# Kernel tuning notes

Hardware: AMD Instinct MI355X
Metric: run time of the kernel (lower is better)

## Reference

```python
import jax, jax.numpy as jnp
import numpy as np

N = 30000        # nodes
E = 600000       # edges
R = 32           # relations
NB = 30          # num_bases
D = 128          # entity_dim == hidden_dim == output_dim
H = 8            # heads, head dim C = D // H = 16
NUM_ENT = 100000
NGRAPH = 16      # graphs in batch
L = 2            # num_rgcn_layers == num_transformer_layers
EPS = 1e-5


def _ln(x, g, b):
    mu = x.mean(-1, keepdims=True)
    var = ((x - mu) ** 2).mean(-1, keepdims=True)
    return (x - mu) * jax.lax.rsqrt(var + EPS) * g + b


def setup_inputs() -> dict:
    key = jax.random.key(0)
    ks = iter(jax.random.split(key, 48))

    def nrm(shape, s=0.05):
        return jax.random.normal(next(ks), shape, jnp.float32) * s

    inp = {}
    inp["node_ids"] = jax.random.randint(next(ks), (N,), 0, NUM_ENT)
    inp["edge_index"] = jax.random.randint(next(ks), (2, E), 0, N)
    inp["edge_type"] = jax.random.randint(next(ks), (E,), 0, R)
    inp["batch"] = jnp.sort(jax.random.randint(next(ks), (N,), 0, NGRAPH))
    inp["entity_emb"] = nrm((NUM_ENT, D)).at[0].set(0.0)  # padding_idx=0
    inp["rel_emb"] = nrm((R, D)).at[0].set(0.0)           # padding_idx=0
    inp["rgcn_comp"] = nrm((L, R, NB))
    inp["rgcn_bases"] = nrm((L, NB, D, D))
    inp["rgcn_root"] = nrm((L, D, D))
    inp["rgcn_bias"] = jnp.zeros((L, D), jnp.float32)
    inp["rgcn_ln_g"] = jnp.ones((L, D), jnp.float32)
    inp["rgcn_ln_b"] = jnp.zeros((L, D), jnp.float32)
    inp["tr_wq"] = nrm((L, D, D)); inp["tr_bq"] = jnp.zeros((L, D), jnp.float32)
    inp["tr_wk"] = nrm((L, D, D)); inp["tr_bk"] = jnp.zeros((L, D), jnp.float32)
    inp["tr_wv"] = nrm((L, D, D)); inp["tr_bv"] = jnp.zeros((L, D), jnp.float32)
    inp["tr_we"] = nrm((L, D, D))                          # lin_edge (bias=False in PyG)
    inp["tr_wskip"] = nrm((L, D, D)); inp["tr_bskip"] = jnp.zeros((L, D), jnp.float32)
    inp["tr_ln_g"] = jnp.ones((L, D), jnp.float32)
    inp["tr_ln_b"] = jnp.zeros((L, D), jnp.float32)
    return inp


def reference(node_ids, edge_index, edge_type, batch, entity_emb, rel_emb,
              rgcn_comp, rgcn_bases, rgcn_root, rgcn_bias, rgcn_ln_g, rgcn_ln_b,
              tr_wq, tr_bq, tr_wk, tr_bk, tr_wv, tr_bv, tr_we, tr_wskip, tr_bskip,
              tr_ln_g, tr_ln_b):
    src, tgt = edge_index[0], edge_index[1]
    C = D // H
    x = entity_emb[node_ids]            # [N, D]
    edge_attr = rel_emb[edge_type]      # [E, D]

    # ---- RGCN layers: basis decomposition, mean aggregation per (target, relation) ----
    seg = tgt * R + edge_type
    cnt = jax.ops.segment_sum(jnp.ones((E,), jnp.float32), seg, num_segments=N * R)
    inv = jnp.where(cnt > 0, 1.0 / jnp.maximum(cnt, 1.0), 0.0)   # [N*R]
    for l in range(L):
        agg = jax.ops.segment_sum(x[src], seg, num_segments=N * R)   # [N*R, D]
        agg = (agg * inv[:, None]).reshape(N, R, D)
        w = jnp.einsum('rb,bio->rio', rgcn_comp[l], rgcn_bases[l])   # [R, D, D]
        x = jnp.einsum('nri,rio->no', agg, w) + x @ rgcn_root[l] + rgcn_bias[l]
        x = jax.nn.relu(_ln(x, rgcn_ln_g[l], rgcn_ln_b[l]))          # dropout = identity (eval)

    # ---- TransformerConv layers: edge-conditioned multi-head attention ----
    for l in range(L):
        q = (x @ tr_wq[l] + tr_bq[l]).reshape(N, H, C)
        k = (x @ tr_wk[l] + tr_bk[l]).reshape(N, H, C)
        v = (x @ tr_wv[l] + tr_bv[l]).reshape(N, H, C)
        e = (edge_attr @ tr_we[l]).reshape(E, H, C)
        kj = k[src] + e                                              # [E, H, C]
        vj = v[src] + e
        alpha = jnp.einsum('ehc,ehc->eh', q[tgt], kj) / np.float32(np.sqrt(C))
        m = jax.ops.segment_max(alpha, tgt, num_segments=N)          # [N, H]
        a = jnp.exp(alpha - m[tgt])
        denom = jax.ops.segment_sum(a, tgt, num_segments=N)
        a = a / jnp.maximum(denom[tgt], 1e-16)                       # softmax per target node
        out = jax.ops.segment_sum((vj * a[:, :, None]).reshape(E, D), tgt, num_segments=N)
        out = out + x @ tr_wskip[l] + tr_bskip[l]                    # root/skip connection
        out = jax.nn.relu(_ln(out, tr_ln_g[l], tr_ln_b[l]))          # dropout = identity (eval)
        x = x + out                                                  # dims match -> residual

    cnt_g = jax.ops.segment_sum(jnp.ones((N,), jnp.float32), batch, num_segments=NGRAPH)
    graph_emb = jax.ops.segment_sum(x, batch, num_segments=NGRAPH) / jnp.maximum(cnt_g, 1.0)[:, None]
    return x, graph_emb
```

## Files before the change

kernel.cpp:

```cpp
#include <hip/hip_runtime.h>

#define NN 30000
#define NE 600000
#define RR 32
#define NBASE 30
#define NG 16

typedef long long i64;
typedef unsigned short ushort;
typedef short bf16x8 __attribute__((ext_vector_type(8)));
typedef float f32x4 __attribute__((ext_vector_type(4)));

__device__ __forceinline__ ushort f2bf(float f){
  unsigned u = __float_as_uint(f);
  u += 0x7fffu + ((u >> 16) & 1u);
  return (ushort)(u >> 16);
}
__device__ __forceinline__ float bf2f(ushort u){
  return __uint_as_float(((unsigned)u) << 16);
}
__device__ __forceinline__ unsigned pk2(float a, float b){
  return (unsigned)f2bf(a) | ((unsigned)f2bf(b) << 16);
}

__global__ void k_gather(const float* __restrict__ emb, const int* __restrict__ ids,
                         float* __restrict__ x, ushort* __restrict__ xb){
  int t = blockIdx.x*256 + threadIdx.x;
  if (t >= NN*32) return;
  int n = t >> 5, c = t & 31;
  float4 v = ((const float4*)emb)[(i64)ids[n]*32 + c];
  ((float4*)x)[(i64)n*32 + c] = v;
  *(uint2*)&xb[(i64)n*128 + c*4] = make_uint2(pk2(v.x, v.y), pk2(v.z, v.w));
}

__global__ void k_cnt(const int* __restrict__ tgt, const int* __restrict__ ety,
                      float* __restrict__ cnt){
  int e = blockIdx.x*256 + threadIdx.x;
  if (e >= NE) return;
  atomicAdd(&cnt[(i64)tgt[e]*RR + ety[e]], 1.0f);
}

__global__ void k_hist_blk(const int* __restrict__ ety, int* __restrict__ hist){
  __shared__ int lh[RR];
  if (threadIdx.x < RR) lh[threadIdx.x] = 0;
  __syncthreads();
  int e0 = blockIdx.x*2048 + threadIdx.x;
  #pragma unroll
  for (int i = 0; i < 8; i++){
    int e = e0 + i*256;
    if (e < NE) atomicAdd(&lh[ety[e]], 1);
  }
  __syncthreads();
  if (threadIdx.x < RR){
    int v = lh[threadIdx.x];
    if (v) atomicAdd(&hist[threadIdx.x], v);
  }
}

__global__ void k_scan(const int* __restrict__ hist, int* __restrict__ base,
                       int* __restrict__ cursor, int* __restrict__ pb,
                       int* __restrict__ pb64){
  if (threadIdx.x != 0 || blockIdx.x != 0) return;
  int s = 0, p = 0, p64 = 0;
  for (int r = 0; r < RR; r++){
    base[r] = s; cursor[r] = s; pb[r] = p; pb64[r] = p64;
    s += hist[r]; p += (hist[r] + 127) >> 7; p64 += (hist[r] + 63) >> 6;
  }
  base[RR] = s; pb[RR] = p; pb64[RR] = p64;
}

__global__ __launch_bounds__(256) void k_scatter_blk(const int* __restrict__ ety,
    int* __restrict__ cursor, int* __restrict__ eord){
  __shared__ int lh[RR];
  __shared__ int lb[RR];
  if (threadIdx.x < RR) lh[threadIdx.x] = 0;
  __syncthreads();
  int e0 = blockIdx.x*2048 + threadIdx.x;
  #pragma unroll
  for (int i = 0; i < 8; i++){
    int e = e0 + i*256;
    if (e < NE) atomicAdd(&lh[ety[e]], 1);
  }
  __syncthreads();
  if (threadIdx.x < RR){
    int c = lh[threadIdx.x];
    lb[threadIdx.x] = c ? atomicAdd(&cursor[threadIdx.x], c) : 0;
  }
  __syncthreads();
  if (threadIdx.x < RR) lh[threadIdx.x] = 0;
  __syncthreads();
  #pragma unroll
  for (int i = 0; i < 8; i++){
    int e = e0 + i*256;
    if (e < NE){
      int r = ety[e];
      int loc = atomicAdd(&lh[r], 1);
      eord[lb[r] + loc] = e;
    }
  }
}

__global__ void k_hist2(const int* __restrict__ etgt, int* __restrict__ hist2){
  int e = blockIdx.x*256 + threadIdx.x;
  if (e >= NE) return;
  atomicAdd(&hist2[etgt[e]], 1);
}

__global__ __launch_bounds__(1024) void k_scan2(const int* __restrict__ hist2,
    int* __restrict__ rowptr, int* __restrict__ cursor2){
  __shared__ int s[1024];
  int t = threadIdx.x;
  int base = t*30;
  int loc[30];
  int sum = 0;
  #pragma unroll
  for (int i = 0; i < 30; i++){
    int v = (base+i < NN) ? hist2[base+i] : 0;
    loc[i] = sum; sum += v;
  }
  s[t] = sum; __syncthreads();
  for (int off = 1; off < 1024; off <<= 1){
    int v = (t >= off) ? s[t-off] : 0;
    __syncthreads();
    s[t] += v;
    __syncthreads();
  }
  int excl = (t > 0) ? s[t-1] : 0;
  #pragma unroll
  for (int i = 0; i < 30; i++){
    int idx = base + i;
    if (idx <= NN){
      rowptr[idx] = excl + loc[i];
      if (idx < NN) cursor2[idx] = excl + loc[i];
    }
  }
}

__global__ void k_scatter2(const int* __restrict__ etgt, const int* __restrict__ esrc,
                           const int* __restrict__ ety, int* __restrict__ cursor2,
                           int2* __restrict__ se2, int* __restrict__ pos2){
  int e = blockIdx.x*256 + threadIdx.x;
  if (e >= NE) return;
  int q = atomicAdd(&cursor2[etgt[e]], 1);
  se2[q] = make_int2(esrc[e], ety[e]);
  pos2[e] = q;
}

__global__ void k_prep(const int* __restrict__ eord, const int* __restrict__ esrc,
                       const int* __restrict__ etgt, const int* __restrict__ ety,
                       const int* __restrict__ pos2, const float* __restrict__ cnt,
                       int* __restrict__ sg_src, int* __restrict__ sg_p2,
                       float* __restrict__ sg_inv){
  int s = blockIdx.x*256 + threadIdx.x;
  if (s >= NE) return;
  int eid = eord[s];
  sg_src[s] = esrc[eid];
  sg_p2[s]  = pos2[eid];
  sg_inv[s] = 1.0f / cnt[(i64)etgt[eid]*RR + ety[eid]];
}

__global__ void k_basis(const float* __restrict__ comp, const float* __restrict__ bases,
                        float* __restrict__ wT, ushort* __restrict__ wTb){
  int t = blockIdx.x*256 + threadIdx.x;
  int r = t >> 14, rem = t & 16383, c = rem >> 7, kk = rem & 127;
  float acc = 0.f;
  for (int b = 0; b < NBASE; b++)
    acc += comp[r*NBASE + b] * bases[(i64)b*16384 + kk*128 + c];
  wT[t] = acc;
  wTb[t] = f2bf(acc);
}

__global__ void k_tw(const float* __restrict__ root, const float* __restrict__ wq,
                     const float* __restrict__ wk, const float* __restrict__ wv,
                     const float* __restrict__ wsk, ushort* __restrict__ out){
  int z = blockIdx.y;
  const float* srcs[5] = {root, wq, wk, wv, wsk};
  const float* S = srcs[z >> 1] + (i64)(z & 1)*16384;
  int idx = blockIdx.x*256 + threadIdx.x;
  int c = idx >> 7, kk = idx & 127;
  out[(i64)z*16384 + idx] = f2bf(S[kk*128 + c]);
}


__global__ __launch_bounds__(256, 4) void k_mm_mfma(const ushort* __restrict__ xb,
    const ushort* __restrict__ wTb, const float* __restrict__ bias,
    float* __restrict__ Y, int nrows){
  __shared__ ushort Xs[16384];
  int t = threadIdx.x;
  int row0 = blockIdx.x * 128;
  for (int i = t; i < 2048; i += 256){
    int row = i >> 4, c = i & 15;
    int gr = min(row0 + row, nrows - 1);
    *(uint4*)((char*)Xs + row*256 + ((c*16) ^ ((row&7)<<4))) =
        *(const uint4*)((const char*)(xb + (i64)gr*128) + c*16);
  }
  __syncthreads();
  int w = t >> 6, l = t & 63;
  int wm = w >> 1, wn = w & 1;
  int lrow = l & 15, lg = l >> 4;
  int swz = (lrow & 7) << 4;
  const char* pX = (const char*)Xs + (wm*64 + lrow)*256;
  const char* pW = (const char*)wTb + (wn*64 + lrow)*256 + 16*lg;
  f32x4 acc[4][4] = {};
  #pragma unroll
  for (int ks = 0; ks < 4; ks++){
    int kb = (16*lg + 64*ks) ^ swz;
    bf16x8 a[4], bx[4];
    #pragma unroll
    for (int ns = 0; ns < 4; ns++) a[ns]  = *(const bf16x8*)(pW + ns*4096 + 64*ks);
    #pragma unroll
    for (int ms = 0; ms < 4; ms++) bx[ms] = *(const bf16x8*)(pX + ms*4096 + kb);
    #pragma unroll
    for (int ms = 0; ms < 4; ms++)
      #pragma unroll
      for (int ns = 0; ns < 4; ns++)
        acc[ms][ns] = __builtin_amdgcn_mfma_f32_16x16x32_bf16(a[ns], bx[ms], acc[ms][ns], 0, 0, 0);
  }
  #pragma unroll
  for (int ms = 0; ms < 4; ms++){
    int m = row0 + wm*64 + ms*16 + lrow;
    if (m >= nrows) continue;
    #pragma unroll
    for (int ns = 0; ns < 4; ns++){
      int n0 = wn*64 + ns*16 + 4*lg;
      float4 bv = *(const float4*)&bias[n0];
      f32x4 v = acc[ms][ns];
      *(float4*)&Y[(i64)m*128 + n0] =
          make_float4(v[0]+bv.x, v[1]+bv.y, v[2]+bv.z, v[3]+bv.w);
    }
  }
}

__global__ __launch_bounds__(256, 4) void k_mm4(const ushort* __restrict__ xb,
    const ushort* __restrict__ wTb, int layer,
    const float* __restrict__ biq, const float* __restrict__ bik,
    const float* __restrict__ biv, const float* __restrict__ bisk,
    ushort* __restrict__ qo, ushort* __restrict__ ko, ushort* __restrict__ vo,
    float* __restrict__ z, int nrows){
  __shared__ ushort Xs[16384];
  int t = threadIdx.x;
  int row0 = blockIdx.x * 128;
  for (int i = t; i < 2048; i += 256){
    int row = i >> 4, c = i & 15;
    int gr = min(row0 + row, nrows - 1);
    *(uint4*)((char*)Xs + row*256 + ((c*16) ^ ((row&7)<<4))) =
        *(const uint4*)((const char*)(xb + (i64)gr*128) + c*16);
  }
  __syncthreads();
  int w = t >> 6, l = t & 63;
  int wm = w >> 1, wn = w & 1;
  int lrow = l & 15, lg = l >> 4;
  int swz = (lrow & 7) << 4;
  const char* pX = (const char*)Xs + (wm*64 + lrow)*256;
  const float* biases[4] = {biq, bik, biv, bisk};
  ushort* outs[3] = {qo, ko, vo};
  #pragma unroll 1
  for (int arr = 0; arr < 4; arr++){
    const char* pW = (const char*)(wTb + (i64)(2 + 2*arr + layer)*16384)
                     + (wn*64 + lrow)*256 + 16*lg;
    f32x4 acc[4][4] = {};
    #pragma unroll
    for (int ks = 0; ks < 4; ks++){
      int kb = (16*lg + 64*ks) ^ swz;
      bf16x8 a[4], bx[4];
      #pragma unroll
      for (int ns = 0; ns < 4; ns++) a[ns]  = *(const bf16x8*)(pW + ns*4096 + 64*ks);
      #pragma unroll
      for (int ms = 0; ms < 4; ms++) bx[ms] = *(const bf16x8*)(pX + ms*4096 + kb);
      #pragma unroll
      for (int ms = 0; ms < 4; ms++)
        #pragma unroll
        for (int ns = 0; ns < 4; ns++)
          acc[ms][ns] = __builtin_amdgcn_mfma_f32_16x16x32_bf16(a[ns], bx[ms], acc[ms][ns], 0, 0, 0);
    }
    const float* bias = biases[arr];
    #pragma unroll
    for (int ms = 0; ms < 4; ms++){
      int m = row0 + wm*64 + ms*16 + lrow;
      if (m >= nrows) continue;
      #pragma unroll
      for (int ns = 0; ns < 4; ns++){
        int n0 = wn*64 + ns*16 + 4*lg;
        float4 bv = *(const float4*)&bias[n0];
        f32x4 v = acc[ms][ns];
        if (arr < 3){
          *(uint2*)&outs[arr][(i64)m*128 + n0] =
              make_uint2(pk2(v[0]+bv.x, v[1]+bv.y), pk2(v[2]+bv.z, v[3]+bv.w));
        } else {
          *(float4*)&z[(i64)m*128 + n0] =
              make_float4(v[0]+bv.x, v[1]+bv.y, v[2]+bv.z, v[3]+bv.w);
        }
      }
    }
  }
}

__global__ __launch_bounds__(256, 4) void k_edge_mfma(
    const int* __restrict__ sg_src, const int* __restrict__ sg_p2,
    const float* __restrict__ sg_inv, const int* __restrict__ hist,
    const int* __restrict__ base, const int* __restrict__ pb,
    const ushort* __restrict__ xb, const ushort* __restrict__ wb,
    ushort* __restrict__ y){
  __shared__ ushort Xs[16384];
  __shared__ int s_src[128];
  __shared__ int s_p2[128];
  __shared__ float s_inv[128];
  int b = blockIdx.x;
  int r = -1;
  #pragma unroll 1
  for (int i = 0; i < RR; i++){
    if (b >= pb[i] && b < pb[i+1]) { r = i; break; }
  }
  if (r < 0) return;
  int chunk = b - pb[r];
  int rowbase = base[r] + chunk*128;
  int nvalid = min(128, hist[r] - chunk*128);
  int t = threadIdx.x;
  if (t < 128){
    bool valid = t < nvalid;
    int slot = rowbase + (valid ? t : 0);
    s_src[t] = sg_src[slot];
    s_p2[t]  = valid ? sg_p2[slot] : NE;
    s_inv[t] = valid ? sg_inv[slot] : 0.0f;
  }
  __syncthreads();
  for (int i = t; i < 2048; i += 256){
    int row = i >> 4, c = i & 15;
    *(uint4*)((char*)Xs + row*256 + ((c*16) ^ ((row&7)<<4))) =
        *(const uint4*)((const char*)(xb + (i64)s_src[row]*128) + c*16);
  }
  __syncthreads();
  int w = t >> 6, l = t & 63;
  int wm = w >> 1, wn = w & 1;
  int lrow = l & 15, lg = l >> 4;
  int swz = (lrow & 7) << 4;
  const char* pX = (const char*)Xs + (wm*64 + lrow)*256;
  const char* pW = (const char*)(wb + (i64)r*16384) + (wn*64 + lrow)*256 + 16*lg;
  f32x4 acc[4][4] = {};
  #pragma unroll
  for (int ks = 0; ks < 4; ks++){
    int kb = (16*lg + 64*ks) ^ swz;
    bf16x8 a[4], bx[4];
    #pragma unroll
    for (int ns = 0; ns < 4; ns++) a[ns]  = *(const bf16x8*)(pW + ns*4096 + 64*ks);
    #pragma unroll
    for (int ms = 0; ms < 4; ms++) bx[ms] = *(const bf16x8*)(pX + ms*4096 + kb);
    #pragma unroll
    for (int ms = 0; ms < 4; ms++)
      #pragma unroll
      for (int ns = 0; ns < 4; ns++)
        acc[ms][ns] = __builtin_amdgcn_mfma_f32_16x16x32_bf16(a[ns], bx[ms], acc[ms][ns], 0, 0, 0);
  }
  __syncthreads();
  #pragma unroll
  for (int ms = 0; ms < 4; ms++){
    int m = wm*64 + ms*16 + lrow;
    float sc = s_inv[m];
    int msk = (m & 7) << 4;
    #pragma unroll
    for (int ns = 0; ns < 4; ns++){
      int n0 = wn*64 + ns*16 + 4*lg;
      f32x4 v = acc[ms][ns];
      *(uint2*)((char*)Xs + m*256 + ((n0*2) ^ msk)) =
          make_uint2(pk2(v[0]*sc, v[1]*sc), pk2(v[2]*sc, v[3]*sc));
    }
  }
  __syncthreads();
  for (int i = t; i < 2048; i += 256){
    int row = i >> 4, c = i & 15;
    uint4 v = *(const uint4*)((const char*)Xs + row*256 + ((c*16) ^ ((row&7)<<4)));
    *(uint4*)&y[(i64)s_p2[row]*128 + c*8] = v;
  }
}

__global__ __launch_bounds__(256) void k_edge_atomic(const int* __restrict__ esrc,
    const int* __restrict__ etgt, const int* __restrict__ eord,
    const int* __restrict__ hist, const int* __restrict__ base,
    const int* __restrict__ pb, const float* __restrict__ cnt,
    const float* __restrict__ x, const float* __restrict__ wT,
    float* __restrict__ z){
  __shared__ float Xs[64][132];
  __shared__ int s_src[64];
  __shared__ int s_tgt[64];
  __shared__ float s_inv[64];
  int b = blockIdx.x;
  int r = -1;
  #pragma unroll 1
  for (int i = 0; i < RR; i++){
    if (b >= pb[i] && b < pb[i+1]) { r = i; break; }
  }
  if (r < 0) return;
  int chunk = b - pb[r];
  int rowbase = base[r] + chunk*64;
  int cnt_r = hist[r];
  if (threadIdx.x < 64){
    int i = threadIdx.x;
    bool valid = (chunk*64 + i) < cnt_r;
    int eid = valid ? eord[rowbase + i] : 0;
    int sv = valid ? esrc[eid] : 0;
    int tv = valid ? etgt[eid] : 0;
    s_src[i] = sv; s_tgt[i] = tv;
    s_inv[i] = valid ? (1.0f / cnt[(i64)tv*RR + r]) : 0.0f;
  }
  __syncthreads();
  for (int idx = threadIdx.x; idx < 64*32; idx += 256){
    int rr = idx >> 5, c4 = idx & 31;
    *(float4*)&Xs[rr][c4*4] = ((const float4*)x)[(i64)s_src[rr]*32 + c4];
  }
  __syncthreads();
  const float* W = wT + (i64)r*16384;
  int m = threadIdx.x & 15, cg = threadIdx.x >> 4;
  float acc[4][8] = {};
  #pragma unroll 2
  for (int k4 = 0; k4 < 128; k4 += 4){
    float4 xv[4], wv[8];
    #pragma unroll
    for (int i = 0; i < 4; i++) xv[i] = *(float4*)&Xs[m + 16*i][k4];
    #pragma unroll
    for (int j = 0; j < 8; j++) wv[j] = *(const float4*)&W[(i64)(cg + 16*j)*128 + k4];
    #pragma unroll
    for (int i = 0; i < 4; i++)
      #pragma unroll
      for (int j = 0; j < 8; j++)
        acc[i][j] += xv[i].x*wv[j].x + xv[i].y*wv[j].y + xv[i].z*wv[j].z + xv[i].w*wv[j].w;
  }
  #pragma unroll
  for (int i = 0; i < 4; i++){
    int rr = m + 16*i;
    float sc = s_inv[rr];
    i64 o = (i64)s_tgt[rr]*128;
    #pragma unroll
    for (int j = 0; j < 8; j++)
      atomicAdd(&z[o + cg + 16*j], acc[i][j]*sc);
  }
}

__global__ void k_seg(const int* __restrict__ rowptr, const ushort* __restrict__ y,
                      const float* __restrict__ z, const float* __restrict__ g,
                      const float* __restrict__ b, float* __restrict__ x,
                      ushort* __restrict__ xb){
  int t = (blockIdx.x*256 + threadIdx.x) >> 6;
  int l = threadIdx.x & 63;
  if (t >= NN) return;
  int q0 = rowptr[t], q1 = rowptr[t+1];
  float ax = 0.f, ay = 0.f;
  for (int q = q0; q < q1; q++){
    ushort2 u = *(const ushort2*)&y[(i64)q*128 + 2*l];
    ax += bf2f(u.x); ay += bf2f(u.y);
  }
  float2 zv = *(const float2*)&z[(i64)t*128 + 2*l];
  float tx = ax + zv.x, ty = ay + zv.y;
  float s = tx + ty;
  #pragma unroll
  for (int o = 1; o < 64; o <<= 1) s += __shfl_xor(s, o);
  float mu = s * 0.0078125f;
  float dx = tx - mu, dy = ty - mu;
  float s2 = dx*dx + dy*dy;
  #pragma unroll
  for (int o = 1; o < 64; o <<= 1) s2 += __shfl_xor(s2, o);
  float rs = rsqrtf(s2 * 0.0078125f + 1e-5f);
  float2 gg = *(const float2*)&g[2*l];
  float2 bb = *(const float2*)&b[2*l];
  float o0 = fmaxf(dx*rs*gg.x + bb.x, 0.f);
  float o1 = fmaxf(dy*rs*gg.y + bb.y, 0.f);
  *(float2*)&x[(i64)t*128 + 2*l] = make_float2(o0, o1);
  *(unsigned*)&xb[(i64)t*128 + 2*l] = pk2(o0, o1);
}

__global__ void k_lnrelu(const float* __restrict__ z, const float* __restrict__ g,
                         const float* __restrict__ b, float* __restrict__ xo,
                         ushort* __restrict__ xb){
  int w = (blockIdx.x*256 + threadIdx.x) >> 6;
  int l = threadIdx.x & 63;
  if (w >= NN) return;
  float2 v = *(const float2*)&z[(i64)w*128 + 2*l];
  float s = v.x + v.y;
  #pragma unroll
  for (int o = 1; o < 64; o <<= 1) s += __shfl_xor(s, o);
  float mu = s * 0.0078125f;
  float dx = v.x - mu, dy = v.y - mu;
  float s2 = dx*dx + dy*dy;
  #pragma unroll
  for (int o = 1; o < 64; o <<= 1) s2 += __shfl_xor(s2, o);
  float rs = rsqrtf(s2 * 0.0078125f + 1e-5f);
  float2 gg = *(const float2*)&g[2*l];
  float2 bb = *(const float2*)&b[2*l];
  float o0 = fmaxf(dx*rs*gg.x + bb.x, 0.f);
  float o1 = fmaxf(dy*rs*gg.y + bb.y, 0.f);
  *(float2*)&xo[(i64)w*128 + 2*l] = make_float2(o0, o1);
  *(unsigned*)&xb[(i64)w*128 + 2*l] = pk2(o0, o1);
}

__global__ void k_ew(const float* __restrict__ rel, const float* __restrict__ we,
                     float* __restrict__ ew){
  int t = blockIdx.x*256 + threadIdx.x;
  int r = t >> 7, c = t & 127;
  float acc = 0.f;
  for (int k = 0; k < 128; k++) acc += rel[r*128 + k] * we[k*128 + c];
  ew[t] = acc;
}

__global__ __launch_bounds__(256) void k_attn(const int2* __restrict__ se2,
    const int* __restrict__ rowptr,
    const ushort* __restrict__ qbb, const ushort* __restrict__ kbb,
    const ushort* __restrict__ vbb, const float* __restrict__ ew,
    const float* __restrict__ sk, const float* __restrict__ g,
    const float* __restrict__ b, float* __restrict__ x, ushort* __restrict__ xb){
  __shared__ float sew[RR*128];
  for (int i = threadIdx.x; i < RR*32; i += 256)
    ((float4*)sew)[i] = ((const float4*)ew)[i];
  __syncthreads();
  int t = (blockIdx.x*256 + threadIdx.x) >> 6;
  int l = threadIdx.x & 63;
  if (t >= NN) return;
  int q0 = rowptr[t], q1 = rowptr[t+1];
  unsigned qu = *(const unsigned*)&qbb[(i64)t*128 + 2*l];
  float qx = bf2f((ushort)qu), qy = bf2f((ushort)(qu >> 16));
  float m = -3.0e38f, den = 0.f, ox = 0.f, oy = 0.f;
  if (q0 < q1){
    int2 sr = se2[q0];
    unsigned ku = *(const unsigned*)&kbb[(i64)sr.x*128 + 2*l];
    unsigned vu = *(const unsigned*)&vbb[(i64)sr.x*128 + 2*l];
    int r = sr.y;
    for (int q = q0; q < q1; q++){
      unsigned kun = 0, vun = 0; int rn = 0;
      if (q + 1 < q1){
        int2 srn = se2[q+1];
        kun = *(const unsigned*)&kbb[(i64)srn.x*128 + 2*l];
        vun = *(const unsigned*)&vbb[(i64)srn.x*128 + 2*l];
        rn = srn.y;
      }
      float2 ev = *(const float2*)&sew[r*128 + 2*l];
      float kx = bf2f((ushort)ku) + ev.x, ky = bf2f((ushort)(ku >> 16)) + ev.y;
      float p = qx*kx + qy*ky;
      p += __shfl_xor(p, 1); p += __shfl_xor(p, 2); p += __shfl_xor(p, 4);
      p *= 0.25f;
      float mn = fmaxf(m, p);
      float scl = __expf(m - mn);
      float wgt = __expf(p - mn);
      den = den*scl + wgt;
      ox = ox*scl + wgt*(bf2f((ushort)vu) + ev.x);
      oy = oy*scl + wgt*(bf2f((ushort)(vu >> 16)) + ev.y);
      m = mn;
      ku = kun; vu = vun; r = rn;
    }
  }
  float dn = fmaxf(den, 1e-16f);
  float2 zv = *(const float2*)&sk[(i64)t*128 + 2*l];
  float tx = ox/dn + zv.x, ty = oy/dn + zv.y;
  float s = tx + ty;
  #pragma unroll
  for (int o = 1; o < 64; o <<= 1) s += __shfl_xor(s, o);
  float mu = s * 0.0078125f;
  float dx = tx - mu, dy = ty - mu;
  float s2 = dx*dx + dy*dy;
  #pragma unroll
  for (int o = 1; o < 64; o <<= 1) s2 += __shfl_xor(s2, o);
  float rs = rsqrtf(s2 * 0.0078125f + 1e-5f);
  float2 gg = *(const float2*)&g[2*l];
  float2 bb = *(const float2*)&b[2*l];
  float o0 = fmaxf(dx*rs*gg.x + bb.x, 0.f);
  float o1 = fmaxf(dy*rs*gg.y + bb.y, 0.f);
  float2 xv = *(const float2*)&x[(i64)t*128 + 2*l];
  float nx = xv.x + o0, ny = xv.y + o1;
  *(float2*)&x[(i64)t*128 + 2*l] = make_float2(nx, ny);
  *(unsigned*)&xb[(i64)t*128 + 2*l] = pk2(nx, ny);
}

__global__ void k_copy(const float* __restrict__ x, float* __restrict__ out){
  int t = blockIdx.x*256 + threadIdx.x;
  if (t >= NN*32) return;
  ((float4*)out)[t] = ((const float4*)x)[t];
}

__global__ void k_cntg(const int* __restrict__ batch, float* __restrict__ cntg){
  __shared__ int lh[NG];
  if (threadIdx.x < NG) lh[threadIdx.x] = 0;
  __syncthreads();
  int n = blockIdx.x*256 + threadIdx.x;
  if (n < NN) atomicAdd(&lh[batch[n]], 1);
  __syncthreads();
  if (threadIdx.x < NG){
    int v = lh[threadIdx.x];
    if (v) atomicAdd(&cntg[threadIdx.x], (float)v);
  }
}

__global__ void k_pool(const float* __restrict__ x, const int* __restrict__ batch,
                       float* __restrict__ gsum){
  __shared__ float acc[NG*128];
  for (int i = threadIdx.x; i < NG*128; i += 256) acc[i] = 0.f;
  __syncthreads();
  int per = (NN + gridDim.x - 1) / gridDim.x;
  int n0 = blockIdx.x*per, n1 = min(n0 + per, NN);
  int sub = threadIdx.x >> 5, c4 = threadIdx.x & 31;
  for (int n = n0 + sub; n < n1; n += 8){
    int g = batch[n];
    float4 xv = ((const float4*)x)[(i64)n*32 + c4];
    atomicAdd(&acc[g*128 + c4*4 + 0], xv.x);
    atomicAdd(&acc[g*128 + c4*4 + 1], xv.y);
    atomicAdd(&acc[g*128 + c4*4 + 2], xv.z);
    atomicAdd(&acc[g*128 + c4*4 + 3], xv.w);
  }
  __syncthreads();
  for (int i = threadIdx.x; i < NG*128; i += 256) atomicAdd(&gsum[i], acc[i]);
}

__global__ void k_poolfin(const float* __restrict__ gsum, const float* __restrict__ cntg,
                          float* __restrict__ gout){
  int t = blockIdx.x*256 + threadIdx.x;
  int g = t >> 7;
  gout[t] = gsum[t] / fmaxf(cntg[g], 1.0f);
}

extern "C" void kernel_launch(void* const* d_in, const int* in_sizes, int n_in,
                              void* d_out, int out_size, void* d_ws, size_t ws_size,
                              hipStream_t stream) {
  const int*   node_ids = (const int*)d_in[0];
  const int*   eidx  = (const int*)d_in[1];
  const int*   esrc  = eidx;
  const int*   etgt  = eidx + NE;
  const int*   ety   = (const int*)d_in[2];
  const int*   batch = (const int*)d_in[3];
  const float* ent   = (const float*)d_in[4];
  const float* rel   = (const float*)d_in[5];
  const float* comp  = (const float*)d_in[6];
  const float* bases = (const float*)d_in[7];
  const float* root  = (const float*)d_in[8];
  const float* rbias = (const float*)d_in[9];
  const float* rlng  = (const float*)d_in[10];
  const float* rlnb  = (const float*)d_in[11];
  const float* wq    = (const float*)d_in[12];
  const float* bq    = (const float*)d_in[13];
  const float* wk    = (const float*)d_in[14];
  const float* bk    = (const float*)d_in[15];
  const float* wv    = (const float*)d_in[16];
  const float* bv    = (const float*)d_in[17];
  const float* we    = (const float*)d_in[18];
  const float* wsk   = (const float*)d_in[19];
  const float* bsk   = (const float*)d_in[20];
  const float* tlng  = (const float*)d_in[21];
  const float* tlnb  = (const float*)d_in[22];
  float* out = (float*)d_out;

  char* wp = (char*)d_ws;
  auto alloc = [&](size_t bytes)->void*{
    void* p = (void*)wp;
    wp += (bytes + 255) & ~(size_t)255;
    return p;
  };
  float*    x     = (float*)alloc((size_t)NN*128*4);
  ushort*   xb    = (ushort*)alloc((size_t)NN*128*2);
  float*    z     = (float*)alloc((size_t)NN*128*4);
  ushort*   qbb   = (ushort*)alloc((size_t)NN*128*2);
  ushort*   kbb   = (ushort*)alloc((size_t)NN*128*2);
  ushort*   vbb   = (ushort*)alloc((size_t)NN*128*2);
  float*    cnt   = (float*)alloc((size_t)NN*RR*4);
  float*    wbT   = (float*)alloc((size_t)RR*16384*4);
  ushort*   wbTb  = (ushort*)alloc((size_t)RR*16384*2);
  ushort*   wTb   = (ushort*)alloc((size_t)10*16384*2);
  float*    ew    = (float*)alloc((size_t)RR*128*4);
  int*      eord  = (int*)alloc((size_t)NE*4);
  int*      pos2  = (int*)alloc((size_t)NE*4);
  int2*     se2   = (int2*)alloc((size_t)NE*8);
  int*      sg_src= (int*)alloc((size_t)NE*4);
  int*      sg_p2 = (int*)alloc((size_t)NE*4);
  float*    sg_inv= (float*)alloc((size_t)NE*4);
  int*      hist  = (int*)alloc(RR*4);
  int*      base  = (int*)alloc((RR+1)*4);
  int*      cursor= (int*)alloc(RR*4);
  int*      pb    = (int*)alloc((RR+1)*4);
  int*      pb64  = (int*)alloc((RR+1)*4);
  int*      hist2 = (int*)alloc((size_t)NN*4);
  int*      rowptr= (int*)alloc((size_t)(NN+1)*4);
  int*      cursor2=(int*)alloc((size_t)NN*4);
  float*    cntg  = (float*)alloc(NG*4);
  float*    gsum  = (float*)alloc((size_t)NG*128*4);
  size_t ybytes = (size_t)(NE + 8)*128*2;
  ushort*   y     = (ushort*)alloc(ybytes);
  bool fast = ((char*)y + ybytes) <= ((char*)d_ws + ws_size);

  dim3 B(256);

  hipMemsetAsync(cnt, 0, (size_t)NN*RR*4, stream);
  hipMemsetAsync(hist, 0, RR*4, stream);
  hipMemsetAsync(hist2, 0, (size_t)NN*4, stream);

  k_gather<<<3750, B, 0, stream>>>(ent, node_ids, x, xb);
  k_cnt<<<2344, B, 0, stream>>>(etgt, ety, cnt);
  k_hist_blk<<<294, B, 0, stream>>>(ety, hist);
  k_scan<<<1, 1, 0, stream>>>(hist, base, cursor, pb, pb64);
  k_scatter_blk<<<294, B, 0, stream>>>(ety, cursor, eord);
  k_hist2<<<2344, B, 0, stream>>>(etgt, hist2);
  k_scan2<<<1, 1024, 0, stream>>>(hist2, rowptr, cursor2);
  k_scatter2<<<2344, B, 0, stream>>>(etgt, esrc, ety, cursor2, se2, pos2);
  k_prep<<<2344, B, 0, stream>>>(eord, esrc, etgt, ety, pos2, cnt, sg_src, sg_p2, sg_inv);
  k_tw<<<dim3(64,10), B, 0, stream>>>(root, wq, wk, wv, wsk, wTb);

  for (int l = 0; l < 2; l++){
    k_basis<<<2048, B, 0, stream>>>(comp + l*RR*NBASE, bases + (i64)l*NBASE*16384, wbT, wbTb);
    k_mm_mfma<<<235, B, 0, stream>>>(xb, wTb + (i64)(0 + l)*16384, rbias + l*128, z, NN);
    if (fast){
      k_edge_mfma<<<4720, B, 0, stream>>>(sg_src, sg_p2, sg_inv, hist, base, pb, xb, wbTb, y);
      k_seg<<<7500, B, 0, stream>>>(rowptr, y, z, rlng + l*128, rlnb + l*128, x, xb);
    } else {
      k_edge_atomic<<<9407, B, 0, stream>>>(esrc, etgt, eord, hist, base, pb64, cnt, x, wbT, z);
      k_lnrelu<<<7500, B, 0, stream>>>(z, rlng + l*128, rlnb + l*128, x, xb);
    }
  }

  for (int l = 0; l < 2; l++){
    k_ew<<<16, B, 0, stream>>>(rel, we + (i64)l*16384, ew);
    k_mm4<<<235, B, 0, stream>>>(xb, wTb, l, bq + l*128, bk + l*128, bv + l*128,
                                 bsk + l*128, qbb, kbb, vbb, z, NN);
    k_attn<<<7500, B, 0, stream>>>(se2, rowptr, qbb, kbb, vbb, ew, z,
                                   tlng + l*128, tlnb + l*128, x, xb);
  }

  k_copy<<<3750, B, 0, stream>>>(x, out);
  hipMemsetAsync(gsum, 0, (size_t)NG*128*4, stream);
  hipMemsetAsync(cntg, 0, NG*4, stream);
  k_cntg<<<118, B, 0, stream>>>(batch, cntg);
  k_pool<<<120, B, 0, stream>>>(x, batch, gsum);
  k_poolfin<<<8, B, 0, stream>>>(gsum, cntg, out + (i64)NN*128);
}
```

Measured before the change: 889.7 us.

## Split attention edge loop across two waves and drop online max rescaling

Each target node's incoming edges are now processed by two wavefronts that take alternate edges, and their partial numerators and denominators are combined through shared memory. This halves the serial dependent chain of gathers per target and doubles the grid. The running max and rescaling of the online softmax are removed, and exp is applied directly to the scaled score. That saves two exps per edge but relies on the scores staying small enough not to overflow. The edge list is padded with two sentinel entries so the next-edge prefetch needs no bounds check.

```diff
diff --git a/kernel.cpp b/kernel.cpp
--- a/kernel.cpp
+++ b/kernel.cpp
@@ -144,6 +144,10 @@
   int q = atomicAdd(&cursor2[etgt[e]], 1);
   se2[q] = make_int2(esrc[e], ety[e]);
   pos2[e] = q;
+  if (e == 0){
+    se2[NE]     = make_int2(0, 0);
+    se2[NE + 1] = make_int2(0, 0);
+  }
 }
 
 __global__ void k_prep(const int* __restrict__ eord, const int* __restrict__ esrc,
@@ -507,44 +511,45 @@
     const float* __restrict__ sk, const float* __restrict__ g,
     const float* __restrict__ b, float* __restrict__ x, ushort* __restrict__ xb){
   __shared__ float sew[RR*128];
+  __shared__ float part[4][3][64];
   for (int i = threadIdx.x; i < RR*32; i += 256)
     ((float4*)sew)[i] = ((const float4*)ew)[i];
   __syncthreads();
-  int t = (blockIdx.x*256 + threadIdx.x) >> 6;
+  int wid = threadIdx.x >> 6;
+  int half = wid & 1;
+  int t = blockIdx.x*2 + (wid >> 1);
   int l = threadIdx.x & 63;
-  if (t >= NN) return;
   int q0 = rowptr[t], q1 = rowptr[t+1];
   unsigned qu = *(const unsigned*)&qbb[(i64)t*128 + 2*l];
-  float qx = bf2f((ushort)qu), qy = bf2f((ushort)(qu >> 16));
-  float m = -3.0e38f, den = 0.f, ox = 0.f, oy = 0.f;
-  if (q0 < q1){
-    int2 sr = se2[q0];
+  float qx = bf2f((ushort)qu) * 0.25f, qy = bf2f((ushort)(qu >> 16)) * 0.25f;
+  float den = 0.f, ox = 0.f, oy = 0.f;
+  int qs = q0 + half;
+  if (qs < q1){
+    int2 sr = se2[qs];
     unsigned ku = *(const unsigned*)&kbb[(i64)sr.x*128 + 2*l];
     unsigned vu = *(const unsigned*)&vbb[(i64)sr.x*128 + 2*l];
     int r = sr.y;
-    for (int q = q0; q < q1; q++){
-      unsigned kun = 0, vun = 0; int rn = 0;
-      if (q + 1 < q1){
-        int2 srn = se2[q+1];
-        kun = *(const unsigned*)&kbb[(i64)srn.x*128 + 2*l];
-        vun = *(const unsigned*)&vbb[(i64)srn.x*128 + 2*l];
-        rn = srn.y;
-      }
+    for (int q = qs; q < q1; q += 2){
+      int2 srn = se2[q + 2];
+      unsigned kun = *(const unsigned*)&kbb[(i64)srn.x*128 + 2*l];
+      unsigned vun = *(const unsigned*)&vbb[(i64)srn.x*128 + 2*l];
       float2 ev = *(const float2*)&sew[r*128 + 2*l];
       float kx = bf2f((ushort)ku) + ev.x, ky = bf2f((ushort)(ku >> 16)) + ev.y;
       float p = qx*kx + qy*ky;
       p += __shfl_xor(p, 1); p += __shfl_xor(p, 2); p += __shfl_xor(p, 4);
-      p *= 0.25f;
-      float mn = fmaxf(m, p);
-      float scl = __expf(m - mn);
-      float wgt = __expf(p - mn);
-      den = den*scl + wgt;
-      ox = ox*scl + wgt*(bf2f((ushort)vu) + ev.x);
-      oy = oy*scl + wgt*(bf2f((ushort)(vu >> 16)) + ev.y);
-      m = mn;
-      ku = kun; vu = vun; r = rn;
+      float wgt = __expf(p);
+      den += wgt;
+      ox += wgt*(bf2f((ushort)vu) + ev.x);
+      oy += wgt*(bf2f((ushort)(vu >> 16)) + ev.y);
+      ku = kun; vu = vun; r = srn.y;
     }
   }
+  part[wid][0][l] = ox; part[wid][1][l] = oy; part[wid][2][l] = den;
+  __syncthreads();
+  if (half) return;
+  ox  += part[wid^1][0][l];
+  oy  += part[wid^1][1][l];
+  den += part[wid^1][2][l];
   float dn = fmaxf(den, 1e-16f);
   float2 zv = *(const float2*)&sk[(i64)t*128 + 2*l];
   float tx = ox/dn + zv.x, ty = oy/dn + zv.y;
@@ -662,7 +667,7 @@
   float*    ew    = (float*)alloc((size_t)RR*128*4);
   int*      eord  = (int*)alloc((size_t)NE*4);
   int*      pos2  = (int*)alloc((size_t)NE*4);
-  int2*     se2   = (int2*)alloc((size_t)NE*8);
+  int2*     se2   = (int2*)alloc((size_t)(NE + 2)*8);
   int*      sg_src= (int*)alloc((size_t)NE*4);
   int*      sg_p2 = (int*)alloc((size_t)NE*4);
   float*    sg_inv= (float*)alloc((size_t)NE*4);
@@ -713,8 +718,8 @@
     k_ew<<<16, B, 0, stream>>>(rel, we + (i64)l*16384, ew);
     k_mm4<<<235, B, 0, stream>>>(xb, wTb, l, bq + l*128, bk + l*128, bv + l*128,
                                  bsk + l*128, qbb, kbb, vbb, z, NN);
-    k_attn<<<7500, B, 0, stream>>>(se2, rowptr, qbb, kbb, vbb, ew, z,
-                                   tlng + l*128, tlnb + l*128, x, xb);
+    k_attn<<<15000, B, 0, stream>>>(se2, rowptr, qbb, kbb, vbb, ew, z,
+                                    tlng + l*128, tlnb + l*128, x, xb);
   }
 
   k_copy<<<3750, B, 0, stream>>>(x, out);
```

After: 899.1 us. About the same (+1.1%).
